# Performance work log

Hardware: AMD Instinct MI355X
Metric: run time of the kernel (lower is better)

The kernel has to match this reference:

```python
import jax, jax.numpy as jnp
import numpy as np

B, S, D, Q, U = 32, 8192, 256, 256, 128


def setup_inputs() -> dict:
    key = jax.random.key(0)
    k1, k2, k3, k4, k5 = jax.random.split(key, 5)
    query = jax.random.normal(k1, (B, Q), dtype=jnp.float32)
    values = jax.random.normal(k2, (B, S, D), dtype=jnp.float32)
    # Dense kernels (Keras stores as [in, out]); scale ~ Glorot-ish
    W1 = jax.random.normal(k3, (D, U), dtype=jnp.float32) * 0.05
    W2 = jax.random.normal(k4, (Q, U), dtype=jnp.float32) * 0.05
    V = jax.random.normal(k5, (U, 1), dtype=jnp.float32) * 0.05
    return {"query": query, "values": values, "W1": W1, "W2": W2, "V": V}


def reference(query, values, W1, W2, V):
    # score = V^T tanh(W1*values + W2*query)  -> (B, S, 1)
    proj_v = jnp.einsum('bsd,du->bsu', values, W1)          # (B,S,U)
    proj_q = jnp.einsum('bq,qu->bu', query, W2)[:, None, :]  # (B,1,U)
    score = jnp.einsum('bsu,uo->bso', jnp.tanh(proj_v + proj_q), V)  # (B,S,1)
    attention_weights = jax.nn.softmax(score, axis=1)        # softmax over seq_len
    # dropout is identity at inference (training=False)
    context = jnp.sum(attention_weights * values, axis=1)    # (B,D)
    return context, attention_weights
```

## Files before the change

### kernel.cpp

```cpp
#include <hip/hip_runtime.h>
#include <stdint.h>

#define B_ 32
#define S_ 8192
#define D_ 256
#define Q_ 256
#define U_ 128

typedef float floatx4 __attribute__((ext_vector_type(4)));
typedef float f32x4 __attribute__((ext_vector_type(4)));
typedef __bf16 bf16x8 __attribute__((ext_vector_type(8)));
typedef unsigned short ushortx4 __attribute__((ext_vector_type(4)));

static __device__ __forceinline__ unsigned short f2bf(float f) {
    unsigned int x = __builtin_bit_cast(unsigned int, f);
    x += 0x7FFFu + ((x >> 16) & 1u);
    return (unsigned short)(x >> 16);
}

static __device__ __forceinline__ float fast_tanh(float x) {
    x = fminf(15.f, fmaxf(-15.f, x));
    float e = __expf(2.f * x);
    return __fdividef(e - 1.f, e + 1.f);
}

__global__ __launch_bounds__(128) void prep_kernel(
        const float* __restrict__ query, const float* __restrict__ W1,
        const float* __restrict__ W2, float* __restrict__ pq,
        unsigned short* __restrict__ w1t) {
    int b = blockIdx.x;
    int t = threadIdx.x;
    __shared__ float qrow[Q_];
    qrow[t] = query[b * Q_ + t];
    qrow[t + 128] = query[b * Q_ + 128 + t];
    __syncthreads();
    float acc = 0.f;
#pragma unroll 8
    for (int q = 0; q < Q_; ++q) acc = fmaf(qrow[q], W2[q * U_ + t], acc);
    pq[b * U_ + t] = acc;
    int base = (b * 128 + t) * 8;
#pragma unroll
    for (int j = 0; j < 8; ++j) {
        int e = base + j;
        int n = e >> 8, k = e & 255;
        w1t[e] = f2bf(W1[k * U_ + n]);
    }
}

__global__ __launch_bounds__(256) void scores_kernel(
        const float* __restrict__ values, const unsigned short* __restrict__ w1t,
        const float* __restrict__ pq, const float* __restrict__ V,
        float* __restrict__ scores) {
    __shared__ unsigned short As[128 * 40];
    __shared__ unsigned short Bs[128 * 40];
    __shared__ float part[256];

    int b = blockIdx.y;
    int s0 = blockIdx.x * 128;
    int tid = threadIdx.x;
    int lane = tid & 63;
    int wave = tid >> 6;
    int wr = wave >> 1, wc = wave & 1;
    int cc = lane & 15, qg = lane >> 4;

    const float* vb = values + ((size_t)b * S_ + s0) * D_;

    f32x4 acc[4][4];
#pragma unroll
    for (int mt = 0; mt < 4; ++mt)
#pragma unroll
        for (int nt = 0; nt < 4; ++nt) acc[mt][nt] = (f32x4){0.f, 0.f, 0.f, 0.f};

    for (int kt = 0; kt < 8; ++kt) {
        int k0 = kt * 32;
        __syncthreads();
#pragma unroll
        for (int i = 0; i < 4; ++i) {
            int idx = tid + i * 256;
            int row = idx >> 3, c = idx & 7;
            floatx4 v = *reinterpret_cast<const floatx4*>(vb + (size_t)row * D_ + k0 + c * 4);
            ushortx4 u;
            u[0] = f2bf(v[0]); u[1] = f2bf(v[1]); u[2] = f2bf(v[2]); u[3] = f2bf(v[3]);
            *reinterpret_cast<ushortx4*>(&As[row * 40 + c * 4]) = u;
            ushortx4 w = *reinterpret_cast<const ushortx4*>(&w1t[row * 256 + k0 + c * 4]);
            *reinterpret_cast<ushortx4*>(&Bs[row * 40 + c * 4]) = w;
        }
        __syncthreads();
        bf16x8 af[4], bfr[4];
#pragma unroll
        for (int mt = 0; mt < 4; ++mt)
            af[mt] = *reinterpret_cast<const bf16x8*>(&As[(wr * 64 + mt * 16 + cc) * 40 + qg * 8]);
#pragma unroll
        for (int nt = 0; nt < 4; ++nt)
            bfr[nt] = *reinterpret_cast<const bf16x8*>(&Bs[(wc * 64 + nt * 16 + cc) * 40 + qg * 8]);
#pragma unroll
        for (int mt = 0; mt < 4; ++mt)
#pragma unroll
            for (int nt = 0; nt < 4; ++nt)
                acc[mt][nt] = __builtin_amdgcn_mfma_f32_16x16x32_bf16(af[mt], bfr[nt], acc[mt][nt], 0, 0, 0);
    }

    float Vu[4], pqu[4];
#pragma unroll
    for (int nt = 0; nt < 4; ++nt) {
        int u = wc * 64 + nt * 16 + cc;
        Vu[nt] = V[u];
        pqu[nt] = pq[b * U_ + u];
    }
#pragma unroll
    for (int mt = 0; mt < 4; ++mt) {
#pragma unroll
        for (int r = 0; r < 4; ++r) {
            float s = 0.f;
#pragma unroll
            for (int nt = 0; nt < 4; ++nt)
                s += Vu[nt] * fast_tanh(acc[mt][nt][r] + pqu[nt]);
            s += __shfl_xor(s, 1);
            s += __shfl_xor(s, 2);
            s += __shfl_xor(s, 4);
            s += __shfl_xor(s, 8);
            if (cc == 0) part[wc * 128 + wr * 64 + mt * 16 + qg * 4 + r] = s;
        }
    }
    __syncthreads();
    if (tid < 128)
        scores[(size_t)b * S_ + s0 + tid] = part[tid] + part[128 + tid];
}

__global__ __launch_bounds__(256) void softmax_kernel(
        const float* __restrict__ scores, float* __restrict__ out) {
    int b = blockIdx.x;
    int tid = threadIdx.x;
    const floatx4* sc = reinterpret_cast<const floatx4*>(scores + (size_t)b * S_);
    floatx4 v[8];
    float m = -1e30f;
#pragma unroll
    for (int i = 0; i < 8; ++i) {
        v[i] = sc[tid + i * 256];
        m = fmaxf(m, fmaxf(fmaxf(v[i][0], v[i][1]), fmaxf(v[i][2], v[i][3])));
    }
#pragma unroll
    for (int off = 32; off >= 1; off >>= 1) m = fmaxf(m, __shfl_xor(m, off));
    __shared__ float red[4];
    __shared__ float red2[4];
    if ((tid & 63) == 0) red[tid >> 6] = m;
    __syncthreads();
    m = fmaxf(fmaxf(red[0], red[1]), fmaxf(red[2], red[3]));
    float lsum = 0.f;
#pragma unroll
    for (int i = 0; i < 8; ++i) {
#pragma unroll
        for (int j = 0; j < 4; ++j) {
            v[i][j] = __expf(v[i][j] - m);
            lsum += v[i][j];
        }
    }
#pragma unroll
    for (int off = 32; off >= 1; off >>= 1) lsum += __shfl_xor(lsum, off);
    if ((tid & 63) == 0) red2[tid >> 6] = lsum;
    __syncthreads();
    float inv = 1.f / (red2[0] + red2[1] + red2[2] + red2[3]);
    floatx4* wout = reinterpret_cast<floatx4*>(out + B_ * D_ + (size_t)b * S_);
#pragma unroll
    for (int i = 0; i < 8; ++i) wout[tid + i * 256] = v[i] * inv;
}

__global__ __launch_bounds__(256) void context_kernel(
        const float* __restrict__ values, const float* __restrict__ weights,
        float* __restrict__ ctx) {
    int b = blockIdx.x;
    int chunk = blockIdx.y;
    int tid = threadIdx.x;
    int g = tid & 63, sub = tid >> 6;
    const float* vb = values + (size_t)b * S_ * D_;
    const float* wb = weights + (size_t)b * S_;
    floatx4 acc = {0.f, 0.f, 0.f, 0.f};
    int s0 = chunk * 256;
    for (int s = s0 + sub; s < s0 + 256; s += 4) {
        float w = wb[s];
        floatx4 v = *reinterpret_cast<const floatx4*>(vb + (size_t)s * D_ + g * 4);
        acc += v * w;
    }
    __shared__ floatx4 cbuf[256];
    cbuf[tid] = acc;
    __syncthreads();
    if (tid < 64) {
        floatx4 r = cbuf[tid] + cbuf[tid + 64] + cbuf[tid + 128] + cbuf[tid + 192];
        atomicAdd(&ctx[b * D_ + g * 4 + 0], r[0]);
        atomicAdd(&ctx[b * D_ + g * 4 + 1], r[1]);
        atomicAdd(&ctx[b * D_ + g * 4 + 2], r[2]);
        atomicAdd(&ctx[b * D_ + g * 4 + 3], r[3]);
    }
}

extern "C" void kernel_launch(void* const* d_in, const int* in_sizes, int n_in,
                              void* d_out, int out_size, void* d_ws, size_t ws_size,
                              hipStream_t stream) {
    const float* query  = (const float*)d_in[0];
    const float* values = (const float*)d_in[1];
    const float* W1     = (const float*)d_in[2];
    const float* W2     = (const float*)d_in[3];
    const float* V      = (const float*)d_in[4];
    float* out = (float*)d_out;

    unsigned short* w1t = (unsigned short*)d_ws;
    float* pq     = (float*)((char*)d_ws + 65536);
    float* scores = (float*)((char*)d_ws + 65536 + 16384);

    hipMemsetAsync(out, 0, B_ * D_ * sizeof(float), stream);

    prep_kernel<<<dim3(32), dim3(128), 0, stream>>>(query, W1, W2, pq, w1t);
    scores_kernel<<<dim3(S_ / 128, B_), dim3(256), 0, stream>>>(values, w1t, pq, V, scores);
    softmax_kernel<<<dim3(B_), dim3(256), 0, stream>>>(scores, out);
    context_kernel<<<dim3(B_, 32), dim3(256), 0, stream>>>(values, out + B_ * D_, out);
}
```

Before: 448.9 us.

## Fuse softmax and context into scores kernel via online-softmax partials

The scores kernel now computes a per-chunk max, exp-sum and unnormalized context partial sum right after the scores, while the chunk's values rows are likely still in cache. A small finalize kernel rescales the chunk partials with the global max and normalizer, and writes the attention weights and the context. This removes the separate softmax pass, the second full read of values in the context kernel, the atomics and the memset. In exchange it adds a per-chunk reduction and partial buffers in workspace.

```diff
diff --git a/kernel.cpp b/kernel.cpp
--- a/kernel.cpp
+++ b/kernel.cpp
@@ -6,6 +6,7 @@
 #define D_ 256
 #define Q_ 256
 #define U_ 128
+#define NCHUNK 64
 
 typedef float floatx4 __attribute__((ext_vector_type(4)));
 typedef float f32x4 __attribute__((ext_vector_type(4)));
@@ -47,16 +48,22 @@
     }
 }
 
-__global__ __launch_bounds__(256) void scores_kernel(
+__global__ __launch_bounds__(256) void fused_kernel(
         const float* __restrict__ values, const unsigned short* __restrict__ w1t,
         const float* __restrict__ pq, const float* __restrict__ V,
-        float* __restrict__ scores) {
+        float* __restrict__ scores, float* __restrict__ mbuf,
+        float* __restrict__ lbuf, float* __restrict__ cpart) {
     __shared__ unsigned short As[128 * 40];
     __shared__ unsigned short Bs[128 * 40];
     __shared__ float part[256];
+    __shared__ float sarr[128];
+    __shared__ float parr[128];
+    __shared__ float redm[1];
+    __shared__ floatx4 cbuf[256];
 
     int b = blockIdx.y;
-    int s0 = blockIdx.x * 128;
+    int cid = blockIdx.x;
+    int s0 = cid * 128;
     int tid = threadIdx.x;
     int lane = tid & 63;
     int wave = tid >> 6;
@@ -123,74 +130,87 @@
         }
     }
     __syncthreads();
-    if (tid < 128)
-        scores[(size_t)b * S_ + s0 + tid] = part[tid] + part[128 + tid];
-}
-
-__global__ __launch_bounds__(256) void softmax_kernel(
-        const float* __restrict__ scores, float* __restrict__ out) {
+    if (tid < 128) {
+        float sc = part[tid] + part[128 + tid];
+        scores[(size_t)b * S_ + s0 + tid] = sc;
+        sarr[tid] = sc;
+    }
+    __syncthreads();
+    if (tid < 64) {
+        float m = fmaxf(sarr[tid], sarr[tid + 64]);
+#pragma unroll
+        for (int off = 32; off >= 1; off >>= 1) m = fmaxf(m, __shfl_xor(m, off));
+        if (tid == 0) redm[0] = m;
+    }
+    __syncthreads();
+    float M = redm[0];
+    if (tid < 128) parr[tid] = __expf(sarr[tid] - M);
+    __syncthreads();
+    if (tid < 64) {
+        float l = parr[tid] + parr[tid + 64];
+#pragma unroll
+        for (int off = 32; off >= 1; off >>= 1) l += __shfl_xor(l, off);
+        if (tid == 0) { mbuf[b * NCHUNK + cid] = M; lbuf[b * NCHUNK + cid] = l; }
+    }
+
+    int g = tid & 63, sub = tid >> 6;
+    floatx4 acc4 = {0.f, 0.f, 0.f, 0.f};
+#pragma unroll 4
+    for (int i = 0; i < 32; ++i) {
+        int r = i * 4 + sub;
+        float w = parr[r];
+        floatx4 v = *reinterpret_cast<const floatx4*>(vb + (size_t)r * D_ + g * 4);
+        acc4 += v * w;
+    }
+    cbuf[tid] = acc4;
+    __syncthreads();
+    if (tid < 64) {
+        floatx4 r4 = cbuf[tid] + cbuf[tid + 64] + cbuf[tid + 128] + cbuf[tid + 192];
+        *reinterpret_cast<floatx4*>(cpart + ((size_t)b * NCHUNK + cid) * D_ + g * 4) = r4;
+    }
+}
+
+__global__ __launch_bounds__(256) void finalize_kernel(
+        const float* __restrict__ scores, const float* __restrict__ mbuf,
+        const float* __restrict__ lbuf, const float* __restrict__ cpart,
+        float* __restrict__ out) {
     int b = blockIdx.x;
     int tid = threadIdx.x;
-    const floatx4* sc = reinterpret_cast<const floatx4*>(scores + (size_t)b * S_);
-    floatx4 v[8];
-    float m = -1e30f;
+    __shared__ float alpha[NCHUNK];
+    __shared__ float MZ[2];
+    if (tid < 64) {
+        float m = mbuf[b * NCHUNK + tid];
+        float l = lbuf[b * NCHUNK + tid];
+        float M = m;
+#pragma unroll
+        for (int off = 32; off >= 1; off >>= 1) M = fmaxf(M, __shfl_xor(M, off));
+        float z = l * __expf(m - M);
+#pragma unroll
+        for (int off = 32; off >= 1; off >>= 1) z += __shfl_xor(z, off);
+        if (tid == 0) { MZ[0] = M; MZ[1] = z; }
+    }
+    __syncthreads();
+    float M = MZ[0];
+    float invZ = 1.f / MZ[1];
+    if (tid < 64) alpha[tid] = __expf(mbuf[b * NCHUNK + tid] - M) * invZ;
+    __syncthreads();
+
+    const floatx4* sc4 = reinterpret_cast<const floatx4*>(scores + (size_t)b * S_);
+    floatx4* w4 = reinterpret_cast<floatx4*>(out + B_ * D_ + (size_t)b * S_);
 #pragma unroll
     for (int i = 0; i < 8; ++i) {
-        v[i] = sc[tid + i * 256];
-        m = fmaxf(m, fmaxf(fmaxf(v[i][0], v[i][1]), fmaxf(v[i][2], v[i][3])));
-    }
-#pragma unroll
-    for (int off = 32; off >= 1; off >>= 1) m = fmaxf(m, __shfl_xor(m, off));
-    __shared__ float red[4];
-    __shared__ float red2[4];
-    if ((tid & 63) == 0) red[tid >> 6] = m;
-    __syncthreads();
-    m = fmaxf(fmaxf(red[0], red[1]), fmaxf(red[2], red[3]));
-    float lsum = 0.f;
-#pragma unroll
-    for (int i = 0; i < 8; ++i) {
-#pragma unroll
-        for (int j = 0; j < 4; ++j) {
-            v[i][j] = __expf(v[i][j] - m);
-            lsum += v[i][j];
-        }
-    }
-#pragma unroll
-    for (int off = 32; off >= 1; off >>= 1) lsum += __shfl_xor(lsum, off);
-    if ((tid & 63) == 0) red2[tid >> 6] = lsum;
-    __syncthreads();
-    float inv = 1.f / (red2[0] + red2[1] + red2[2] + red2[3]);
-    floatx4* wout = reinterpret_cast<floatx4*>(out + B_ * D_ + (size_t)b * S_);
-#pragma unroll
-    for (int i = 0; i < 8; ++i) wout[tid + i * 256] = v[i] * inv;
-}
-
-__global__ __launch_bounds__(256) void context_kernel(
-        const float* __restrict__ values, const float* __restrict__ weights,
-        float* __restrict__ ctx) {
-    int b = blockIdx.x;
-    int chunk = blockIdx.y;
-    int tid = threadIdx.x;
-    int g = tid & 63, sub = tid >> 6;
-    const float* vb = values + (size_t)b * S_ * D_;
-    const float* wb = weights + (size_t)b * S_;
-    floatx4 acc = {0.f, 0.f, 0.f, 0.f};
-    int s0 = chunk * 256;
-    for (int s = s0 + sub; s < s0 + 256; s += 4) {
-        float w = wb[s];
-        floatx4 v = *reinterpret_cast<const floatx4*>(vb + (size_t)s * D_ + g * 4);
-        acc += v * w;
-    }
-    __shared__ floatx4 cbuf[256];
-    cbuf[tid] = acc;
-    __syncthreads();
-    if (tid < 64) {
-        floatx4 r = cbuf[tid] + cbuf[tid + 64] + cbuf[tid + 128] + cbuf[tid + 192];
-        atomicAdd(&ctx[b * D_ + g * 4 + 0], r[0]);
-        atomicAdd(&ctx[b * D_ + g * 4 + 1], r[1]);
-        atomicAdd(&ctx[b * D_ + g * 4 + 2], r[2]);
-        atomicAdd(&ctx[b * D_ + g * 4 + 3], r[3]);
-    }
+        floatx4 v = sc4[tid + i * 256];
+        floatx4 w;
+#pragma unroll
+        for (int j = 0; j < 4; ++j) w[j] = __expf(v[j] - M) * invZ;
+        w4[tid + i * 256] = w;
+    }
+
+    float acc = 0.f;
+#pragma unroll 8
+    for (int c = 0; c < NCHUNK; ++c)
+        acc = fmaf(alpha[c], cpart[((size_t)b * NCHUNK + c) * D_ + tid], acc);
+    out[b * D_ + tid] = acc;
 }
 
 extern "C" void kernel_launch(void* const* d_in, const int* in_sizes, int n_in,
@@ -203,14 +223,16 @@
     const float* V      = (const float*)d_in[4];
     float* out = (float*)d_out;
 
-    unsigned short* w1t = (unsigned short*)d_ws;
-    float* pq     = (float*)((char*)d_ws + 65536);
-    float* scores = (float*)((char*)d_ws + 65536 + 16384);
-
-    hipMemsetAsync(out, 0, B_ * D_ * sizeof(float), stream);
+    char* ws = (char*)d_ws;
+    unsigned short* w1t = (unsigned short*)ws;               ws += 65536;
+    float* pq     = (float*)ws;                              ws += 16384;
+    float* scores = (float*)ws;                              ws += B_ * S_ * 4;
+    float* mbuf   = (float*)ws;                              ws += B_ * NCHUNK * 4;
+    float* lbuf   = (float*)ws;                              ws += B_ * NCHUNK * 4;
+    float* cpart  = (float*)ws;
 
     prep_kernel<<<dim3(32), dim3(128), 0, stream>>>(query, W1, W2, pq, w1t);
-    scores_kernel<<<dim3(S_ / 128, B_), dim3(256), 0, stream>>>(values, w1t, pq, V, scores);
-    softmax_kernel<<<dim3(B_), dim3(256), 0, stream>>>(scores, out);
-    context_kernel<<<dim3(B_, 32), dim3(256), 0, stream>>>(values, out + B_ * D_, out);
-}
+    fused_kernel<<<dim3(NCHUNK, B_), dim3(256), 0, stream>>>(values, w1t, pq, V,
+                                                             scores, mbuf, lbuf, cpart);
+    finalize_kernel<<<dim3(B_), dim3(256), 0, stream>>>(scores, mbuf, lbuf, cpart, out);
+}
```

Result: faster. 428.5 us (-4.5%).
